# Kernel tuning notes

Hardware: AMD Instinct MI355X
Metric: run time of the kernel (lower is better)

The kernel has to match this reference:

```python
import jax, jax.numpy as jnp
import numpy as np

T, D, N, K, H = 4096, 2560, 8, 4, 256
QUERY_PRE_ATTN_SCALAR = 256.0
ROPE_THETA = 10000.0
RMS_EPS = 1e-6
SLIDING_WINDOW = 1024
NEG_INF = -1e30


def setup_inputs() -> dict:
    key = jax.random.key(0)
    ks = jax.random.split(key, 6)
    return {
        "x": jax.random.normal(ks[0], (T, D), dtype=jnp.float32),
        "wq": jax.random.normal(ks[1], (D, N, H), dtype=jnp.float32) * 0.02,
        "wk": jax.random.normal(ks[2], (D, K, H), dtype=jnp.float32) * 0.02,
        "wv": jax.random.normal(ks[3], (D, K, H), dtype=jnp.float32) * 0.02,
        "wo": jax.random.normal(ks[4], (N, H, D), dtype=jnp.float32) * 0.02,
        "q_norm_w": jnp.ones((H,), dtype=jnp.float32),
        "k_norm_w": jnp.ones((H,), dtype=jnp.float32),
        "positions": jnp.arange(T, dtype=jnp.int32),
    }


def rms_norm(x, w, eps=RMS_EPS):
    rms = jnp.sqrt(jnp.mean(x * x, axis=-1, keepdims=True) + eps)
    return w * (x / rms)


def apply_rope(x, positions, head_dim, theta):
    # x: [T, heads, H]; rotate-half RoPE
    half = head_dim // 2
    inv_freq = theta ** (-(jnp.arange(half, dtype=jnp.float32) * 2.0 / head_dim))
    ang = positions.astype(jnp.float32)[:, None] * inv_freq  # [T, half]
    sin = jnp.sin(ang)[:, None, :]
    cos = jnp.cos(ang)[:, None, :]
    x1, x2 = jnp.split(x, 2, axis=-1)
    return jnp.concatenate([x1 * cos - x2 * sin, x2 * cos + x1 * sin], axis=-1)


def reference(x, wq, wk, wv, wo, q_norm_w, k_norm_w, positions):
    # QKV projections (per-head)
    q = jnp.einsum('td,dnh->tnh', x, wq)            # [T, N, H]
    q = rms_norm(q, q_norm_w)
    q = q * (QUERY_PRE_ATTN_SCALAR ** -0.5)
    q = apply_rope(q, positions, H, ROPE_THETA)

    k = jnp.einsum('td,dkh->tkh', x, wk)            # [T, K, H]
    k = rms_norm(k, k_norm_w)
    k = apply_rope(k, positions, H, ROPE_THETA)

    v = jnp.einsum('td,dkh->tkh', x, wv)            # [T, K, H]

    # GQA sliding-window causal attention
    G = N // K
    qh = q.reshape(T, K, G, H)
    scores = jnp.einsum('tkgh,skh->kgts', qh, k)    # [K, G, T, T]
    pq = positions[:, None]
    pk = positions[None, :]
    mask = (pk <= pq) & (pq - pk < SLIDING_WINDOW)  # [T, T]
    scores = jnp.where(mask, scores, NEG_INF)
    p = jax.nn.softmax(scores, axis=-1)
    attn = jnp.einsum('kgts,skh->tkgh', p, v).reshape(T, N, H)

    o = jnp.einsum('tnh,nhd->td', attn, wo)         # [T, D]
    new_kv_cache = jnp.stack([k, v])                # [2, T, K, H]
    return new_kv_cache, o
```

## Files before the change

kernel.cpp:

```cpp
#include <hip/hip_runtime.h>
#include <stdint.h>

#define T_TOK 4096
#define DM    2560
#define NQ    8
#define NKV   4
#define HD    256
#define WIN   1024

using bf16x8 = __attribute__((ext_vector_type(8))) short;
using f32x4  = __attribute__((ext_vector_type(4))) float;
typedef unsigned short u16;

__device__ __forceinline__ u16 f2bf(float x) {
  union { float f; uint32_t u; } v; v.f = x;
  uint32_t u = v.u;
  return (u16)((u + 0x7fffu + ((u >> 16) & 1u)) >> 16);
}
__device__ __forceinline__ float bf2f(u16 b) {
  union { uint32_t u; float f; } v; v.u = ((uint32_t)b) << 16;
  return v.f;
}

__device__ __forceinline__ void async_cp16(const void* g, void* lds) {
  __builtin_amdgcn_global_load_lds(
      (const __attribute__((address_space(1))) uint32_t*)(uintptr_t)g,
      (__attribute__((address_space(3))) uint32_t*)(uint32_t)(uintptr_t)lds,
      16, 0, 0);
}

__global__ __launch_bounds__(256) void prelude(
    const float* __restrict__ x,  const float* __restrict__ wq,
    const float* __restrict__ wk, const float* __restrict__ wv,
    const float* __restrict__ wo,
    u16* __restrict__ xb, u16* __restrict__ wqkvT, u16* __restrict__ woT)
{
  __shared__ u16 tile[64][72];
  const int bid0 = blockIdx.x;

  if (bid0 < 1024) {
    for (int i = (bid0 * 256 + threadIdx.x) * 8; i < T_TOK * DM; i += 1024 * 256 * 8) {
      float4 a = *(const float4*)(x + i);
      float4 b = *(const float4*)(x + i + 4);
      bf16x8 o;
      o[0] = (short)f2bf(a.x); o[1] = (short)f2bf(a.y);
      o[2] = (short)f2bf(a.z); o[3] = (short)f2bf(a.w);
      o[4] = (short)f2bf(b.x); o[5] = (short)f2bf(b.y);
      o[6] = (short)f2bf(b.z); o[7] = (short)f2bf(b.w);
      *(bf16x8*)(xb + i) = o;
    }
    return;
  }

  const float* src; u16* dst; int R, C, bx, by;
  if (bid0 < 2304)      { int b = bid0 - 1024; src = wq; dst = wqkvT;             R = DM;   C = 2048; bx = b & 31; by = b >> 5; }
  else if (bid0 < 2944) { int b = bid0 - 2304; src = wk; dst = wqkvT + 2048 * DM; R = DM;   C = 1024; bx = b & 15; by = b >> 4; }
  else if (bid0 < 3584) { int b = bid0 - 2944; src = wv; dst = wqkvT + 3072 * DM; R = DM;   C = 1024; bx = b & 15; by = b >> 4; }
  else                  { int b = bid0 - 3584; src = wo; dst = woT;               R = 2048; C = DM;   bx = b % 40; by = b / 40; }

  const int r0 = by * 64, c0 = bx * 64;
  const int tr = threadIdx.x >> 6, tc = threadIdx.x & 63;
  #pragma unroll
  for (int i = 0; i < 16; ++i) {
    int r = tr + i * 4;
    tile[r][tc] = f2bf(src[(size_t)(r0 + r) * C + c0 + tc]);
  }
  __syncthreads();
  const int oc = threadIdx.x >> 3, ch = threadIdx.x & 7;
  #pragma unroll
  for (int h = 0; h < 2; ++h) {
    const int c = oc + h * 32;
    bf16x8 v;
    #pragma unroll
    for (int j = 0; j < 8; ++j) v[j] = (short)tile[ch * 8 + j][c];
    *(bf16x8*)(dst + (size_t)(c0 + c) * R + r0 + ch * 8) = v;
  }
}

template<bool F32OUT>
__global__ __launch_bounds__(512, 1) void gemm256p(
    const u16* __restrict__ A, const u16* __restrict__ B, void* __restrict__ Cv,
    int Kd, int lda, int ldb, int ldc)
{
  __shared__ __align__(16) u16 lds[2][2][256 * 64];
  const int tid = threadIdx.x;
  const int wave = tid >> 6, lane = tid & 63;
  const int lg = lane >> 4, lc = lane & 15;
  const int wr = wave >> 2, wc = wave & 3;
  const int nwg = gridDim.x, bid = blockIdx.x;
  const int nid = (bid & 7) * (nwg >> 3) + (bid >> 3);
  const int m0 = (nid & 15) * 256, n0 = (nid >> 4) * 256;
  const int NT = Kd >> 6;

  const int srow = tid >> 3;
  const int scol = ((tid & 7) * 16) ^ ((srow & 7) << 4);
  const u16* Ag = A + (size_t)(m0 + srow) * lda + (scol >> 1);
  const u16* Bg = B + (size_t)(n0 + srow) * ldb + (scol >> 1);

  #define STAGE_B4(BUF, KT) do {                                              \
    const int kc_ = (KT) * 64;                                                \
    _Pragma("unroll")                                                         \
    for (int li = 0; li < 4; ++li)                                            \
      async_cp16(Bg + (size_t)(li * 64) * ldb + kc_,                          \
                 (char*)&lds[BUF][1][0] + li * 8192 + wave * 1024);           \
  } while (0)
  #define STAGE_A2(BUF, KT, H) do {                                           \
    const int kc_ = (KT) * 64;                                                \
    async_cp16(Ag + (size_t)((H) * 64) * lda + kc_,                           \
               (char*)&lds[BUF][0][0] + (H) * 8192 + wave * 1024);            \
    async_cp16(Ag + (size_t)((H) * 64 + 128) * lda + kc_,                     \
               (char*)&lds[BUF][0][0] + ((H) + 2) * 8192 + wave * 1024);      \
  } while (0)
  #define LOAD_AF(P) do {                                                     \
    _Pragma("unroll")                                                         \
    for (int im = 0; im < 2; ++im)                                            \
      _Pragma("unroll")                                                       \
      for (int k2 = 0; k2 < 2; ++k2) {                                        \
        const int row = wr * 128 + ((P) * 2 + im) * 16 + lc;                  \
        const int cb = k2 * 64 + lg * 16;                                     \
        af[im][k2] = *(const bf16x8*)(Ab + row * 128 + (cb ^ ((row & 7) << 4))); \
      }                                                                       \
  } while (0)
  #define MFMA_Q(P) do {                                                      \
    __builtin_amdgcn_s_setprio(1);                                            \
    _Pragma("unroll")                                                         \
    for (int im = 0; im < 2; ++im)                                            \
      _Pragma("unroll")                                                       \
      for (int j = 0; j < 4; ++j)                                             \
        _Pragma("unroll")                                                     \
        for (int k2 = 0; k2 < 2; ++k2)                                        \
          acc[(P) * 2 + im][j] = __builtin_amdgcn_mfma_f32_16x16x32_bf16(     \
              af[im][k2], bfr[j][k2], acc[(P) * 2 + im][j], 0, 0, 0);         \
    __builtin_amdgcn_s_setprio(0);                                            \
  } while (0)
  #define LGKM0_BAR() do {                                                    \
    asm volatile("s_waitcnt lgkmcnt(0)" ::: "memory");                        \
    __builtin_amdgcn_s_barrier();                                             \
    __builtin_amdgcn_sched_barrier(0);                                        \
  } while (0)

  const f32x4 zf = {0.f, 0.f, 0.f, 0.f};
  f32x4 acc[8][4];
  #pragma unroll
  for (int i = 0; i < 8; ++i)
    #pragma unroll
    for (int j = 0; j < 4; ++j) acc[i][j] = zf;

  STAGE_B4(0, 0); STAGE_A2(0, 0, 0); STAGE_A2(0, 0, 1);
  STAGE_B4(1, 1); STAGE_A2(1, 1, 0); STAGE_A2(1, 1, 1);
  asm volatile("s_waitcnt vmcnt(8)" ::: "memory");
  __builtin_amdgcn_s_barrier();
  __builtin_amdgcn_sched_barrier(0);

  for (int t = 0; t < NT; ++t) {
    const int cur = t & 1;
    const char* Ab = (const char*)&lds[cur][0][0];
    const char* Bb = (const char*)&lds[cur][1][0];
    int nk = t + 2; if (nk > NT - 1) nk = NT - 1;

    bf16x8 bfr[4][2], af[2][2];
    #pragma unroll
    for (int j = 0; j < 4; ++j)
      #pragma unroll
      for (int k2 = 0; k2 < 2; ++k2) {
        const int row = wc * 64 + j * 16 + lc;
        const int cb = k2 * 64 + lg * 16;
        bfr[j][k2] = *(const bf16x8*)(Bb + row * 128 + (cb ^ ((row & 7) << 4)));
      }
    LOAD_AF(0);
    LGKM0_BAR();
    STAGE_B4(cur, nk);
    MFMA_Q(0);
    LOAD_AF(1);
    LGKM0_BAR();
    STAGE_A2(cur, nk, 0);
    MFMA_Q(1);
    LOAD_AF(2);
    MFMA_Q(2);
    LOAD_AF(3);
    LGKM0_BAR();
    STAGE_A2(cur, nk, 1);
    MFMA_Q(3);
    asm volatile("s_waitcnt vmcnt(8)" ::: "memory");
    __builtin_amdgcn_s_barrier();
    __builtin_amdgcn_sched_barrier(0);
  }
  #undef STAGE_B4
  #undef STAGE_A2
  #undef LOAD_AF
  #undef MFMA_Q
  #undef LGKM0_BAR

  #pragma unroll
  for (int i = 0; i < 8; ++i)
    #pragma unroll
    for (int j = 0; j < 4; ++j)
      #pragma unroll
      for (int r = 0; r < 4; ++r) {
        const int row = m0 + wr * 128 + i * 16 + lg * 4 + r;
        const int col = n0 + wc * 64 + j * 16 + lc;
        if (F32OUT) ((float*)Cv)[(size_t)row * ldc + col] = acc[i][j][r];
        else        ((u16*)Cv)[(size_t)row * ldc + col] = f2bf(acc[i][j][r]);
      }
}

__global__ __launch_bounds__(512, 1) void gemm_p2(
    const u16* __restrict__ A, const u16* __restrict__ B, float* __restrict__ C,
    int Kd, int lda, int ldb, int ldc)
{
  __shared__ __align__(16) u16 lds[2][(128 + 320) * 64];
  const int tid = threadIdx.x;
  const int wave = tid >> 6, lane = tid & 63;
  const int lg = lane >> 4, lc = lane & 15;
  const int wr = wave >> 2, wc = wave & 3;
  const int nwg = gridDim.x, bid = blockIdx.x;
  const int nid = (bid & 7) * (nwg >> 3) + (bid >> 3);
  const int m0 = (nid & 31) * 128, n0 = (nid >> 5) * 320;
  const int NT = Kd >> 6;

  const int srow = tid >> 3;
  const int scol = ((tid & 7) * 16) ^ ((srow & 7) << 4);
  const u16* Ag = A + (size_t)(m0 + srow) * lda + (scol >> 1);
  const u16* Bg = B + (size_t)(n0 + srow) * ldb + (scol >> 1);

  #define STAGE_B5(BUF, KT) do {                                              \
    const int kc_ = (KT) * 64;                                                \
    _Pragma("unroll")                                                         \
    for (int li = 0; li < 5; ++li)                                            \
      async_cp16(Bg + (size_t)(li * 64) * ldb + kc_,                          \
                 (char*)&lds[BUF][0] + 16384 + li * 8192 + wave * 1024);      \
  } while (0)
  #define STAGE_A2P(BUF, KT) do {                                             \
    const int kc_ = (KT) * 64;                                                \
    _Pragma("unroll")                                                         \
    for (int li = 0; li < 2; ++li)                                            \
      async_cp16(Ag + (size_t)(li * 64) * lda + kc_,                          \
                 (char*)&lds[BUF][0] + li * 8192 + wave * 1024);              \
  } while (0)
  #define LOAD_AF2(P) do {                                                    \
    _Pragma("unroll")                                                         \
    for (int im = 0; im < 2; ++im)                                            \
      _Pragma("unroll")                                                       \
      for (int k2 = 0; k2 < 2; ++k2) {                                        \
        const int row = wr * 64 + ((P) * 2 + im) * 16 + lc;                   \
        const int cb = k2 * 64 + lg * 16;                                     \
        af[im][k2] = *(const bf16x8*)(Ab + row * 128 + (cb ^ ((row & 7) << 4))); \
      }                                                                       \
  } while (0)
  #define MFMA_Q2(P) do {                                                     \
    __builtin_amdgcn_s_setprio(1);                                            \
    _Pragma("unroll")                                                         \
    for (int im = 0; im < 2; ++im)                                            \
      _Pragma("unroll")                                                       \
      for (int j = 0; j < 5; ++j)                                             \
        _Pragma("unroll")                                                     \
        for (int k2 = 0; k2 < 2; ++k2)                                        \
          acc[(P) * 2 + im][j] = __builtin_amdgcn_mfma_f32_16x16x32_bf16(     \
              af[im][k2], bfr[j][k2], acc[(P) * 2 + im][j], 0, 0, 0);         \
    __builtin_amdgcn_s_setprio(0);                                            \
  } while (0)
  #define LGKM0_BAR2() do {                                                   \
    asm volatile("s_waitcnt lgkmcnt(0)" ::: "memory");                        \
    __builtin_amdgcn_s_barrier();                                             \
    __builtin_amdgcn_sched_barrier(0);                                        \
  } while (0)

  const f32x4 zf = {0.f, 0.f, 0.f, 0.f};
  f32x4 acc[4][5];
  #pragma unroll
  for (int i = 0; i < 4; ++i)
    #pragma unroll
    for (int j = 0; j < 5; ++j) acc[i][j] = zf;

  STAGE_B5(0, 0); STAGE_A2P(0, 0);
  STAGE_B5(1, 1); STAGE_A2P(1, 1);
  asm volatile("s_waitcnt vmcnt(7)" ::: "memory");
  __builtin_amdgcn_s_barrier();
  __builtin_amdgcn_sched_barrier(0);

  for (int t = 0; t < NT; ++t) {
    const int cur = t & 1;
    const char* Ab = (const char*)&lds[cur][0];
    const char* Bb = Ab + 16384;
    int nk = t + 2; if (nk > NT - 1) nk = NT - 1;

    bf16x8 bfr[5][2], af[2][2];
    #pragma unroll
    for (int j = 0; j < 5; ++j)
      #pragma unroll
      for (int k2 = 0; k2 < 2; ++k2) {
        const int row = wc * 80 + j * 16 + lc;
        const int cb = k2 * 64 + lg * 16;
        bfr[j][k2] = *(const bf16x8*)(Bb + row * 128 + (cb ^ ((row & 7) << 4)));
      }
    LOAD_AF2(0);
    LGKM0_BAR2();
    STAGE_B5(cur, nk);
    MFMA_Q2(0);
    LOAD_AF2(1);
    LGKM0_BAR2();
    STAGE_A2P(cur, nk);
    MFMA_Q2(1);
    asm volatile("s_waitcnt vmcnt(7)" ::: "memory");
    __builtin_amdgcn_s_barrier();
    __builtin_amdgcn_sched_barrier(0);
  }
  #undef STAGE_B5
  #undef STAGE_A2P
  #undef LOAD_AF2
  #undef MFMA_Q2
  #undef LGKM0_BAR2

  #pragma unroll
  for (int i = 0; i < 4; ++i)
    #pragma unroll
    for (int j = 0; j < 5; ++j)
      #pragma unroll
      for (int r = 0; r < 4; ++r) {
        const int row = m0 + wr * 64 + i * 16 + lg * 4 + r;
        const int col = n0 + wc * 80 + j * 16 + lc;
        C[(size_t)row * ldc + col] = acc[i][j][r];
      }
}

__global__ __launch_bounds__(256) void fuse_norm_rope(
    const u16* __restrict__ qkv, const float* __restrict__ qnw, const float* __restrict__ knw,
    const int* __restrict__ pos, u16* __restrict__ qb, u16* __restrict__ kb,
    u16* __restrict__ vb, float* __restrict__ kvout)
{
  const int t = blockIdx.x;
  const int wave = threadIdx.x >> 6, lane = threadIdx.x & 63;
  const float p = (float)pos[t];
  const float kf = 0.10381025296523007f;
  float s0, c0, s1, c1;
  sincosf(p * exp2f(-(float)lane * kf), &s0, &c0);
  sincosf(p * exp2f(-(float)(lane + 64) * kf), &s1, &c1);
  const u16* row = qkv + (size_t)t * 4096;

  for (int pp = 0; pp < 4; ++pp) {
    const int hr = pp * 4 + wave;
    if (hr >= 12) {
      const int kk = hr - 12;
      const u16* src = row + 3072 + kk * 256;
      float* dstf = kvout + (size_t)T_TOK * NKV * HD + ((size_t)t * NKV + kk) * HD;
      u16*   dstb = vb + ((size_t)t * NKV + kk) * HD;
      #pragma unroll
      for (int q4 = 0; q4 < 4; ++q4) {
        const u16 s = src[lane + q4 * 64];
        dstf[lane + q4 * 64] = bf2f(s);
        dstb[lane + q4 * 64] = s;
      }
    } else {
      const bool isq = hr < 8;
      const int cb = isq ? hr * 256 : 2048 + (hr - 8) * 256;
      float v0 = bf2f(row[cb + lane]);
      float v1 = bf2f(row[cb + lane + 64]);
      float v2 = bf2f(row[cb + lane + 128]);
      float v3 = bf2f(row[cb + lane + 192]);
      float ss = v0 * v0 + v1 * v1 + v2 * v2 + v3 * v3;
      #pragma unroll
      for (int off = 1; off < 64; off <<= 1) ss += __shfl_xor(ss, off);
      float sc = rsqrtf(ss * (1.0f / 256.0f) + 1e-6f);
      if (isq) sc *= 0.0625f;
      const float* wn = isq ? qnw : knw;
      v0 *= sc * wn[lane];
      v1 *= sc * wn[lane + 64];
      v2 *= sc * wn[lane + 128];
      v3 *= sc * wn[lane + 192];
      const float n0 = v0 * c0 - v2 * s0;
      const float n2 = v2 * c0 + v0 * s0;
      const float n1 = v1 * c1 - v3 * s1;
      const float n3 = v3 * c1 + v1 * s1;
      if (isq) {
        u16* dst = qb + (size_t)t * 2048 + hr * 256;
        dst[lane]       = f2bf(n0);
        dst[lane + 64]  = f2bf(n1);
        dst[lane + 128] = f2bf(n2);
        dst[lane + 192] = f2bf(n3);
      } else {
        const int kk = hr - 8;
        float* dstf = kvout + ((size_t)t * NKV + kk) * HD;
        dstf[lane]       = n0;
        dstf[lane + 64]  = n1;
        dstf[lane + 128] = n2;
        dstf[lane + 192] = n3;
        u16* dstb = kb + ((size_t)t * NKV + kk) * HD;
        dstb[lane]       = f2bf(n0);
        dstb[lane + 64]  = f2bf(n1);
        dstb[lane + 128] = f2bf(n2);
        dstb[lane + 192] = f2bf(n3);
      }
    }
  }
}

__global__ __launch_bounds__(256) void transpose_v(
    const u16* __restrict__ vc, u16* __restrict__ vt)
{
  __shared__ u16 tile[64][72];
  const int kk = blockIdx.z;
  const int t0 = blockIdx.y * 64, h0 = blockIdx.x * 64;
  const int lr = threadIdx.x >> 3, ch = threadIdx.x & 7;
  #pragma unroll
  for (int h = 0; h < 2; ++h) {
    const int row = lr + h * 32;
    *(bf16x8*)&tile[row][ch * 8] =
        *(const bf16x8*)&vc[((size_t)(t0 + row) * NKV + kk) * HD + h0 + ch * 8];
  }
  __syncthreads();
  #pragma unroll
  for (int h = 0; h < 2; ++h) {
    const int hc = lr + h * 32;
    bf16x8 v;
    #pragma unroll
    for (int j = 0; j < 8; ++j) v[j] = (short)tile[ch * 8 + j][hc];
    *(bf16x8*)&vt[(size_t)kk * HD * T_TOK + (size_t)(h0 + hc) * T_TOK + t0 + ch * 8] = v;
  }
}

__global__ __launch_bounds__(512, 1) void attn_kernel(
    const u16* __restrict__ qb, const u16* __restrict__ kc,
    const u16* __restrict__ vt, u16* __restrict__ ob)
{
  __shared__ __align__(16) u16 Ks[2][64 * 256];
  __shared__ __align__(16) u16 Vts[2][256 * 64];
  __shared__ __align__(16) u16 Ps[8][16 * 64];

  const int bid = blockIdx.x;
  const int xcd = bid & 7, idx = bid >> 3;
  const int kk = xcd >> 1;
  const int t0 = (idx + (xcd & 1) * 32) * 64;
  const int tid = threadIdx.x;
  const int wave = tid >> 6, lane = tid & 63;
  const int lg = lane >> 4, lc = lane & 15;
  const int hq = kk * 2 + (wave >> 2);
  const int wrow = (wave & 3) * 16;
  const int lswz = (lc & 7) << 4;
  const f32x4 zf = {0.f, 0.f, 0.f, 0.f};

  const int lrowK = tid >> 5;
  const int scolK = ((tid & 31) * 16) ^ ((lrowK & 7) << 4);
  const int lrowV = tid >> 3;
  const int scolV = ((tid & 7) * 16) ^ ((lrowV & 7) << 4);

  #define STAGEKV(KT, BUF) do {                                                \
    const int kb_ = (KT) * 64;                                                 \
    const u16* kp_ = kc + (size_t)(kb_ + lrowK) * (NKV * HD) + kk * HD + (scolK >> 1); \
    _Pragma("unroll")                                                          \
    for (int is = 0; is < 4; ++is)                                             \
      async_cp16(kp_ + (size_t)(is * 16) * (NKV * HD),                         \
                 (char*)&Ks[BUF][0] + is * 8192 + wave * 1024);                \
    const u16* vp_ = vt + (size_t)kk * (HD * T_TOK) + (size_t)lrowV * T_TOK + kb_ + (scolV >> 1); \
    _Pragma("unroll")                                                          \
    for (int is = 0; is < 4; ++is)                                             \
      async_cp16(vp_ + (size_t)(is * 64) * T_TOK,                              \
                 (char*)&Vts[BUF][0] + is * 8192 + wave * 1024);               \
  } while (0)

  bf16x8 qf[8];
  {
    const u16* qp = qb + (size_t)(t0 + wrow + lc) * 2048 + hq * 256 + lg * 8;
    #pragma unroll
    for (int ks = 0; ks < 8; ++ks) qf[ks] = *(const bf16x8*)(qp + ks * 32);
  }

  f32x4 o_acc[16];
  #pragma unroll
  for (int j = 0; j < 16; ++j) o_acc[j] = zf;
  float m_r[4], l_r[4];
  #pragma unroll
  for (int r = 0; r < 4; ++r) { m_r[r] = -1e30f; l_r[r] = 0.f; }

  const int mtile = t0 >> 6;
  const int ktf = (mtile >= 16) ? (mtile - 16) : 0;

  STAGEKV(ktf, 0);
  __syncthreads();

  int cur = 0;
  for (int kt = ktf; kt <= mtile; ++kt) {
    const int kb = kt * 64;
    if (kt < mtile) STAGEKV(kt + 1, cur ^ 1);

    const u16* Kb = &Ks[cur][0];
    const u16* Vb = &Vts[cur][0];

    f32x4 sf[4];
    #pragma unroll
    for (int j = 0; j < 4; ++j) sf[j] = zf;
    __builtin_amdgcn_s_setprio(1);
    #pragma unroll
    for (int ks = 0; ks < 8; ++ks)
      #pragma unroll
      for (int j = 0; j < 4; ++j) {
        const int row = j * 16 + lc;
        bf16x8 kf = *(const bf16x8*)((const char*)Kb + ((row * 512 + ks * 64 + lg * 16) ^ lswz));
        sf[j] = __builtin_amdgcn_mfma_f32_16x16x32_bf16(qf[ks], kf, sf[j], 0, 0, 0);
      }
    __builtin_amdgcn_s_setprio(0);

    const bool interior = (kb >= t0 - 960) && (kb <= t0 - 64);
    if (!interior) {
      #pragma unroll
      for (int j = 0; j < 4; ++j) {
        const int gcol = kb + j * 16 + lc;
        #pragma unroll
        for (int r = 0; r < 4; ++r) {
          const int grow = t0 + wrow + lg * 4 + r;
          if ((unsigned)(grow - gcol) >= WIN) sf[j][r] = -1e30f;
        }
      }
    }

    float a_r[4];
    #pragma unroll
    for (int r = 0; r < 4; ++r) {
      float v = fmaxf(fmaxf(sf[0][r], sf[1][r]), fmaxf(sf[2][r], sf[3][r]));
      v = fmaxf(v, __shfl_xor(v, 1));
      v = fmaxf(v, __shfl_xor(v, 2));
      v = fmaxf(v, __shfl_xor(v, 4));
      v = fmaxf(v, __shfl_xor(v, 8));
      const float mn = fmaxf(m_r[r], v);
      a_r[r] = __expf(m_r[r] - mn);
      m_r[r] = mn;
    }

    char* myP = (char*)&Ps[wave][0];
    #pragma unroll
    for (int r = 0; r < 4; ++r) {
      const int row = lg * 4 + r;
      const int rsw = (row & 7) << 4;
      float su = 0.f;
      #pragma unroll
      for (int j = 0; j < 4; ++j) {
        const float p = __expf(sf[j][r] - m_r[r]);
        su += p;
        *(u16*)(myP + ((row * 128 + (j * 16 + lc) * 2) ^ rsw)) = f2bf(p);
      }
      su += __shfl_xor(su, 1);
      su += __shfl_xor(su, 2);
      su += __shfl_xor(su, 4);
      su += __shfl_xor(su, 8);
      l_r[r] = l_r[r] * a_r[r] + su;
    }

    #pragma unroll
    for (int j = 0; j < 16; ++j) {
      o_acc[j][0] *= a_r[0];
      o_acc[j][1] *= a_r[1];
      o_acc[j][2] *= a_r[2];
      o_acc[j][3] *= a_r[3];
    }

    bf16x8 pa[2];
    #pragma unroll
    for (int ks = 0; ks < 2; ++ks)
      pa[ks] = *(const bf16x8*)(myP + ((lc * 128 + ks * 64 + lg * 16) ^ lswz));
    __builtin_amdgcn_s_setprio(1);
    #pragma unroll
    for (int ks = 0; ks < 2; ++ks)
      #pragma unroll
      for (int j = 0; j < 16; ++j) {
        const int row = j * 16 + lc;
        bf16x8 vf = *(const bf16x8*)((const char*)Vb + ((row * 128 + ks * 64 + lg * 16) ^ lswz));
        o_acc[j] = __builtin_amdgcn_mfma_f32_16x16x32_bf16(pa[ks], vf, o_acc[j], 0, 0, 0);
      }
    __builtin_amdgcn_s_setprio(0);

    __syncthreads();
    cur ^= 1;
  }
  #undef STAGEKV

  #pragma unroll
  for (int r = 0; r < 4; ++r) {
    const float li = 1.f / l_r[r];
    const size_t rowb = (size_t)(t0 + wrow + lg * 4 + r) * 2048 + hq * 256 + lc;
    #pragma unroll
    for (int j = 0; j < 16; ++j)
      ob[rowb + j * 16] = f2bf(o_acc[j][r] * li);
  }
}

extern "C" void kernel_launch(void* const* d_in, const int* in_sizes, int n_in,
                              void* d_out, int out_size, void* d_ws, size_t ws_size,
                              hipStream_t stream)
{
  (void)in_sizes; (void)n_in; (void)out_size; (void)ws_size;
  const float* x   = (const float*)d_in[0];
  const float* wq  = (const float*)d_in[1];
  const float* wk  = (const float*)d_in[2];
  const float* wv  = (const float*)d_in[3];
  const float* wo  = (const float*)d_in[4];
  const float* qnw = (const float*)d_in[5];
  const float* knw = (const float*)d_in[6];
  const int*   pos = (const int*)d_in[7];
  float* out = (float*)d_out;

  char* ws = (char*)d_ws;
  u16* woT   = (u16*)(ws);
  u16* xb    = (u16*)(ws + 10485760);
  u16* wqkvT = (u16*)(ws + 31457280);
  u16* qkv   = (u16*)(ws + 52428800);
  u16* q_b   = xb;
  u16* kb    = wqkvT;
  u16* vb    = (u16*)(ws + 31457280 + 8388608);
  u16* vtb   = qkv;
  u16* attn  = (u16*)(ws + 52428800 + 8388608);

  prelude<<<4864, 256, 0, stream>>>(x, wq, wk, wv, wo, xb, wqkvT, woT);

  gemm256p<false><<<256, 512, 0, stream>>>(xb, wqkvT, qkv, DM, DM, DM, 4096);

  fuse_norm_rope<<<T_TOK, 256, 0, stream>>>(qkv, qnw, knw, pos, q_b, kb, vb, out);

  transpose_v<<<dim3(4, 64, 4), 256, 0, stream>>>(vb, vtb);

  attn_kernel<<<256, 512, 0, stream>>>(q_b, kb, vtb, attn);

  gemm_p2<<<256, 512, 0, stream>>>(attn, woT, out + 2 * (size_t)T_TOK * NKV * HD,
                                   2048, 2048, 2048, DM);
}
```

Before: 239.3 us.

## Fuse RMS-norm and RoPE epilogue into QKV projection GEMM

The separate fuse_norm_rope kernel is removed, and the QKV GEMM epilogue now does the per-head RMS norm, query scaling, RoPE and the V copy directly from the accumulators. Row sums of squares are reduced through shuffles and LDS, and the rotate-half partner values are exchanged through the reused LDS tile. This drops one kernel launch and the bf16 qkv intermediate round trip through global memory, and it also keeps K and V in fp32 before rounding. In exchange the epilogue is heavier: sincosf is computed per element, the stores are strided, and only half the waves do the RoPE stores. Workspace buffers are re-laid out to avoid aliasing.

```diff
diff --git a/kernel.cpp b/kernel.cpp
--- a/kernel.cpp
+++ b/kernel.cpp
@@ -77,12 +77,16 @@
   }
 }
 
-template<bool F32OUT>
-__global__ __launch_bounds__(512, 1) void gemm256p(
-    const u16* __restrict__ A, const u16* __restrict__ B, void* __restrict__ Cv,
-    int Kd, int lda, int ldb, int ldc)
+__global__ __launch_bounds__(512, 1) void gemm_qkv(
+    const u16* __restrict__ A, const u16* __restrict__ B,
+    const float* __restrict__ qnw, const float* __restrict__ knw,
+    const int* __restrict__ pos,
+    u16* __restrict__ qb, u16* __restrict__ kb, u16* __restrict__ vb,
+    float* __restrict__ kvout, int Kd, int lda, int ldb)
 {
   __shared__ __align__(16) u16 lds[2][2][256 * 64];
+  __shared__ float partial[4][256];
+  __shared__ float scl[256];
   const int tid = threadIdx.x;
   const int wave = tid >> 6, lane = tid & 63;
   const int lg = lane >> 4, lc = lane & 15;
@@ -191,17 +195,105 @@
   #undef MFMA_Q
   #undef LGKM0_BAR
 
+  const int g = nid >> 4;
+
+  if (g >= 12) {
+    const int kkh = g - 12;
+    #pragma unroll
+    for (int i = 0; i < 8; ++i)
+      #pragma unroll
+      for (int r = 0; r < 4; ++r) {
+        const int t = m0 + wr * 128 + i * 16 + lg * 4 + r;
+        #pragma unroll
+        for (int j = 0; j < 4; ++j) {
+          const int h = wc * 64 + j * 16 + lc;
+          const float v = acc[i][j][r];
+          kvout[(size_t)T_TOK * NKV * HD + ((size_t)t * NKV + kkh) * HD + h] = v;
+          vb[((size_t)t * NKV + kkh) * HD + h] = f2bf(v);
+        }
+      }
+    return;
+  }
+
   #pragma unroll
   for (int i = 0; i < 8; ++i)
     #pragma unroll
-    for (int j = 0; j < 4; ++j)
+    for (int r = 0; r < 4; ++r) {
+      float s = acc[i][0][r] * acc[i][0][r] + acc[i][1][r] * acc[i][1][r]
+              + acc[i][2][r] * acc[i][2][r] + acc[i][3][r] * acc[i][3][r];
+      s += __shfl_xor(s, 1); s += __shfl_xor(s, 2);
+      s += __shfl_xor(s, 4); s += __shfl_xor(s, 8);
+      if (lc == 0) partial[wc][wr * 128 + i * 16 + lg * 4 + r] = s;
+    }
+  __syncthreads();
+  if (tid < 256) {
+    const float ss = partial[0][tid] + partial[1][tid] + partial[2][tid] + partial[3][tid];
+    scl[tid] = rsqrtf(ss * (1.0f / 256.0f) + 1e-6f);
+  }
+  __syncthreads();
+
+  const bool isq = (g < 8);
+  const float qsc = isq ? 0.0625f : 1.0f;
+  const float* wn = isq ? qnw : knw;
+  float wnv[4];
+  #pragma unroll
+  for (int j = 0; j < 4; ++j) wnv[j] = wn[wc * 64 + j * 16 + lc] * qsc;
+  #pragma unroll
+  for (int i = 0; i < 8; ++i)
+    #pragma unroll
+    for (int r = 0; r < 4; ++r) {
+      const float sc = scl[wr * 128 + i * 16 + lg * 4 + r];
+      #pragma unroll
+      for (int j = 0; j < 4; ++j) acc[i][j][r] *= sc * wnv[j];
+    }
+
+  float* ldsF = (float*)&lds[0][0][0];
+  if (wc >= 2) {
+    #pragma unroll
+    for (int i = 0; i < 8; ++i)
       #pragma unroll
       for (int r = 0; r < 4; ++r) {
-        const int row = m0 + wr * 128 + i * 16 + lg * 4 + r;
-        const int col = n0 + wc * 64 + j * 16 + lc;
-        if (F32OUT) ((float*)Cv)[(size_t)row * ldc + col] = acc[i][j][r];
-        else        ((u16*)Cv)[(size_t)row * ldc + col] = f2bf(acc[i][j][r]);
-      }
+        const int row = wr * 128 + i * 16 + lg * 4 + r;
+        #pragma unroll
+        for (int j = 0; j < 4; ++j)
+          ldsF[row * 128 + (wc - 2) * 64 + j * 16 + lc] = acc[i][j][r];
+      }
+  }
+  __syncthreads();
+
+  if (wc < 2) {
+    const float kf = 0.10381025296523007f;
+    #pragma unroll
+    for (int i = 0; i < 8; ++i)
+      #pragma unroll
+      for (int r = 0; r < 4; ++r) {
+        const int row = wr * 128 + i * 16 + lg * 4 + r;
+        const int t = m0 + row;
+        const float p = (float)pos[t];
+        #pragma unroll
+        for (int j = 0; j < 4; ++j) {
+          const int h = wc * 64 + j * 16 + lc;
+          const float x1 = acc[i][j][r];
+          const float x2 = ldsF[row * 128 + h];
+          float sn, cs;
+          sincosf(p * exp2f(-(float)h * kf), &sn, &cs);
+          const float o1 = x1 * cs - x2 * sn;
+          const float o2 = x2 * cs + x1 * sn;
+          if (isq) {
+            qb[(size_t)t * 2048 + g * 256 + h]       = f2bf(o1);
+            qb[(size_t)t * 2048 + g * 256 + h + 128] = f2bf(o2);
+          } else {
+            const int kkh = g - 8;
+            float* kf32 = kvout + ((size_t)t * NKV + kkh) * HD;
+            kf32[h]       = o1;
+            kf32[h + 128] = o2;
+            u16* kb16 = kb + ((size_t)t * NKV + kkh) * HD;
+            kb16[h]       = f2bf(o1);
+            kb16[h + 128] = f2bf(o2);
+          }
+        }
+      }
+  }
 }
 
 __global__ __launch_bounds__(512, 1) void gemm_p2(
@@ -321,77 +413,6 @@
         const int col = n0 + wc * 80 + j * 16 + lc;
         C[(size_t)row * ldc + col] = acc[i][j][r];
       }
-}
-
-__global__ __launch_bounds__(256) void fuse_norm_rope(
-    const u16* __restrict__ qkv, const float* __restrict__ qnw, const float* __restrict__ knw,
-    const int* __restrict__ pos, u16* __restrict__ qb, u16* __restrict__ kb,
-    u16* __restrict__ vb, float* __restrict__ kvout)
-{
-  const int t = blockIdx.x;
-  const int wave = threadIdx.x >> 6, lane = threadIdx.x & 63;
-  const float p = (float)pos[t];
-  const float kf = 0.10381025296523007f;
-  float s0, c0, s1, c1;
-  sincosf(p * exp2f(-(float)lane * kf), &s0, &c0);
-  sincosf(p * exp2f(-(float)(lane + 64) * kf), &s1, &c1);
-  const u16* row = qkv + (size_t)t * 4096;
-
-  for (int pp = 0; pp < 4; ++pp) {
-    const int hr = pp * 4 + wave;
-    if (hr >= 12) {
-      const int kk = hr - 12;
-      const u16* src = row + 3072 + kk * 256;
-      float* dstf = kvout + (size_t)T_TOK * NKV * HD + ((size_t)t * NKV + kk) * HD;
-      u16*   dstb = vb + ((size_t)t * NKV + kk) * HD;
-      #pragma unroll
-      for (int q4 = 0; q4 < 4; ++q4) {
-        const u16 s = src[lane + q4 * 64];
-        dstf[lane + q4 * 64] = bf2f(s);
-        dstb[lane + q4 * 64] = s;
-      }
-    } else {
-      const bool isq = hr < 8;
-      const int cb = isq ? hr * 256 : 2048 + (hr - 8) * 256;
-      float v0 = bf2f(row[cb + lane]);
-      float v1 = bf2f(row[cb + lane + 64]);
-      float v2 = bf2f(row[cb + lane + 128]);
-      float v3 = bf2f(row[cb + lane + 192]);
-      float ss = v0 * v0 + v1 * v1 + v2 * v2 + v3 * v3;
-      #pragma unroll
-      for (int off = 1; off < 64; off <<= 1) ss += __shfl_xor(ss, off);
-      float sc = rsqrtf(ss * (1.0f / 256.0f) + 1e-6f);
-      if (isq) sc *= 0.0625f;
-      const float* wn = isq ? qnw : knw;
-      v0 *= sc * wn[lane];
-      v1 *= sc * wn[lane + 64];
-      v2 *= sc * wn[lane + 128];
-      v3 *= sc * wn[lane + 192];
-      const float n0 = v0 * c0 - v2 * s0;
-      const float n2 = v2 * c0 + v0 * s0;
-      const float n1 = v1 * c1 - v3 * s1;
-      const float n3 = v3 * c1 + v1 * s1;
-      if (isq) {
-        u16* dst = qb + (size_t)t * 2048 + hr * 256;
-        dst[lane]       = f2bf(n0);
-        dst[lane + 64]  = f2bf(n1);
-        dst[lane + 128] = f2bf(n2);
-        dst[lane + 192] = f2bf(n3);
-      } else {
-        const int kk = hr - 8;
-        float* dstf = kvout + ((size_t)t * NKV + kk) * HD;
-        dstf[lane]       = n0;
-        dstf[lane + 64]  = n1;
-        dstf[lane + 128] = n2;
-        dstf[lane + 192] = n3;
-        u16* dstb = kb + ((size_t)t * NKV + kk) * HD;
-        dstb[lane]       = f2bf(n0);
-        dstb[lane + 64]  = f2bf(n1);
-        dstb[lane + 128] = f2bf(n2);
-        dstb[lane + 192] = f2bf(n3);
-      }
-    }
-  }
 }
 
 __global__ __launch_bounds__(256) void transpose_v(
@@ -601,18 +622,16 @@
   u16* woT   = (u16*)(ws);
   u16* xb    = (u16*)(ws + 10485760);
   u16* wqkvT = (u16*)(ws + 31457280);
-  u16* qkv   = (u16*)(ws + 52428800);
-  u16* q_b   = xb;
-  u16* kb    = wqkvT;
-  u16* vb    = (u16*)(ws + 31457280 + 8388608);
-  u16* vtb   = qkv;
-  u16* attn  = (u16*)(ws + 52428800 + 8388608);
+  u16* q_b   = (u16*)(ws + 52428800);
+  u16* kb    = (u16*)(ws + 69206016);
+  u16* vb    = (u16*)(ws + 77594624);
+  u16* vtb   = xb;
+  u16* attn  = wqkvT;
 
   prelude<<<4864, 256, 0, stream>>>(x, wq, wk, wv, wo, xb, wqkvT, woT);
 
-  gemm256p<false><<<256, 512, 0, stream>>>(xb, wqkvT, qkv, DM, DM, DM, 4096);
-
-  fuse_norm_rope<<<T_TOK, 256, 0, stream>>>(qkv, qnw, knw, pos, q_b, kb, vb, out);
+  gemm_qkv<<<256, 512, 0, stream>>>(xb, wqkvT, qnw, knw, pos,
+                                    q_b, kb, vb, out, DM, DM, DM);
 
   transpose_v<<<dim3(4, 64, 4), 256, 0, stream>>>(vb, vtb);
 
```

After: 302.0 us. 1.26x slower.
